# Kernel tuning notes

Hardware: AMD Instinct MI355X
Metric: run time of the kernel (lower is better)

The kernel has to match this reference:

```python
import jax, jax.numpy as jnp
import numpy as np

D = 512          # descriptor_dim
H = 8            # num_heads
HD = D // H      # per-head dim
L = 12           # GNN layers: ['self','cross']*6
NAMES = ['self', 'cross'] * 6
SINKHORN_ITERS = 100
IN_EPS = 1e-5    # InstanceNorm1d eps


def _conv1x1(W, b, x):
    # W: [o, d], b: [o], x: [b, d, n] -> [b, o, n]  (1x1 Conv1d)
    return jnp.einsum('od,bdn->bon', W, x) + b[:, None]


def _instance_norm(x):
    # InstanceNorm1d(affine=False): normalize each (batch, channel) over n
    mean = jnp.mean(x, axis=-1, keepdims=True)
    var = jnp.mean(jnp.square(x - mean), axis=-1, keepdims=True)  # biased
    return (x - mean) * jax.lax.rsqrt(var + IN_EPS)


def _mha(x, src, Wq, bq, Wk, bk, Wv, bv, Wm, bm):
    # x, src: [b, D, n] / [b, D, m]; fused head-major QKV projections
    b, _, n = x.shape
    m = src.shape[2]
    q = _conv1x1(Wq, bq, x).reshape(b, H, HD, n)
    k = _conv1x1(Wk, bk, src).reshape(b, H, HD, m)
    v = _conv1x1(Wv, bv, src).reshape(b, H, HD, m)
    scores = jnp.einsum('bhdn,bhdm->bhnm', q, k) / np.float32(np.sqrt(HD))
    prob = jax.nn.softmax(scores, axis=-1)
    out = jnp.einsum('bhnm,bhdm->bhdn', prob, v)      # [b, h, hd, n]
    # torch stacks heads at dim=2 -> [b, hd, h, n], then views (b, hd*h, n):
    out = out.transpose(0, 2, 1, 3).reshape(b, D, n)  # dim-major merge order
    return _conv1x1(Wm, bm, out)


def _prop_layer(x, src, Wq, bq, Wk, bk, Wv, bv, Wm, bm, W1, b1, W2, b2):
    # AttentionalPropagation: attn message + MLP([2D, 2D, D]) with InstanceNorm
    msg = _mha(x, src, Wq, bq, Wk, bk, Wv, bv, Wm, bm)
    y = jnp.concatenate([x, msg], axis=1)             # [b, 2D, n]
    z = jax.nn.relu(_instance_norm(_conv1x1(W1, b1, y)))
    return _conv1x1(W2, b2, z)                        # [b, D, n]


def _log_optimal_transport(scores, alpha, iters):
    b, m, n = scores.shape
    ms = jnp.asarray(m, scores.dtype)
    ns = jnp.asarray(n, scores.dtype)
    bins0 = jnp.broadcast_to(alpha, (b, m, 1))
    bins1 = jnp.broadcast_to(alpha, (b, 1, n))
    a = jnp.broadcast_to(alpha, (b, 1, 1))
    couplings = jnp.concatenate(
        [jnp.concatenate([scores, bins0], -1),
         jnp.concatenate([bins1, a], -1)], 1)         # [b, m+1, n+1]
    norm = -jnp.log(ms + ns)
    log_mu = jnp.concatenate([jnp.full((m,), norm), (jnp.log(ns) + norm)[None]])
    log_nu = jnp.concatenate([jnp.full((n,), norm), (jnp.log(ms) + norm)[None]])
    log_mu = jnp.broadcast_to(log_mu, (b, m + 1))
    log_nu = jnp.broadcast_to(log_nu, (b, n + 1))

    def step(carry, _):
        u, v = carry
        u = log_mu - jax.scipy.special.logsumexp(couplings + v[:, None, :], axis=2)
        v = log_nu - jax.scipy.special.logsumexp(couplings + u[:, :, None], axis=1)
        return (u, v), None

    (u, v), _ = jax.lax.scan(
        step, (jnp.zeros_like(log_mu), jnp.zeros_like(log_nu)), None,
        length=iters)
    return couplings + u[:, :, None] + v[:, None, :] - norm


def setup_inputs() -> dict:
    key = jax.random.key(0)
    ks = jax.random.split(key, 12)
    B, N0, N1 = 4, 1024, 1024
    s = np.float32(0.03)  # ~1/sqrt(D) init scale for stability over 12 layers

    def p(k, shape):
        return jax.random.normal(k, shape, jnp.float32) * s

    return {
        'descs_0': jax.random.normal(ks[0], (B, N0, D), jnp.float32),
        'descs_1': jax.random.normal(ks[1], (B, N1, D), jnp.float32),
        'Wq': p(ks[2], (L, D, D)), 'bq': jnp.zeros((L, D), jnp.float32),
        'Wk': p(ks[3], (L, D, D)), 'bk': jnp.zeros((L, D), jnp.float32),
        'Wv': p(ks[4], (L, D, D)), 'bv': jnp.zeros((L, D), jnp.float32),
        'Wm': p(ks[5], (L, D, D)), 'bm': jnp.zeros((L, D), jnp.float32),
        'W1': p(ks[6], (L, 2 * D, 2 * D)), 'b1': jnp.zeros((L, 2 * D), jnp.float32),
        'W2': p(ks[7], (L, D, 2 * D)), 'b2': jnp.zeros((L, D), jnp.float32),
        'Wf': p(ks[8], (D, D)), 'bf': jnp.zeros((D,), jnp.float32),
        'bin_score': jnp.asarray(1.0, jnp.float32),
    }


def reference(descs_0, descs_1, Wq, bq, Wk, bk, Wv, bv, Wm, bm,
              W1, b1, W2, b2, Wf, bf, bin_score):
    # [B, N, D] -> channels-first [B, D, N]
    x0 = jnp.transpose(descs_0, (0, 2, 1))
    x1 = jnp.transpose(descs_1, (0, 2, 1))
    for i, name in enumerate(NAMES):
        s0, s1 = (x1, x0) if name == 'cross' else (x0, x1)
        args = (Wq[i], bq[i], Wk[i], bk[i], Wv[i], bv[i], Wm[i], bm[i],
                W1[i], b1[i], W2[i], b2[i])
        d0 = _prop_layer(x0, s0, *args)
        d1 = _prop_layer(x1, s1, *args)
        x0 = x0 + d0
        x1 = x1 + d1
    m0 = _conv1x1(Wf, bf, x0)
    m1 = _conv1x1(Wf, bf, x1)
    scores = jnp.einsum('bdn,bdm->bnm', m0, m1) / np.float32(np.sqrt(D))
    return _log_optimal_transport(scores, bin_score, SINKHORN_ITERS)
```

## Files before the change

### kernel.cpp

```cpp
#include <hip/hip_runtime.h>
#include <hip/hip_bf16.h>
#include <hip/hip_fp16.h>
#include <cmath>

using bf16 = __hip_bfloat16;
typedef __attribute__((ext_vector_type(8))) short short8;
typedef __attribute__((ext_vector_type(4))) short shortx4;
typedef __attribute__((ext_vector_type(4))) float floatx4;
typedef unsigned long long u64t;

__device__ __forceinline__ void lds_load16(void* lds, const void* g) {
  __builtin_amdgcn_global_load_lds(
      (const __attribute__((address_space(1))) void*)g,
      (__attribute__((address_space(3))) void*)lds, 16, 0, 0);
}

struct GemmP {
  const bf16* A; const bf16* B;
  int M, N, K, lda, ldb;
  long sAimg, sAh, sBimg, sBh;
  int ZH, cross;
  float scale;
  const float* bias;
  float* Cf; int ldcf; long sCfImg, sCfH;
  bf16* Cb; int ldcb; long sCbImg, sCbH;
  __half* Ch; int ldch; long sChImg, sChH;
  const float* resid;
  bf16* Cv; int vColOfs;
  float* statsOut;
};

template <int NTILE>
__global__ __launch_bounds__(256, 2)
void gemm_bt(GemmP p) {
  __shared__ __align__(16) bf16 As[128 * 32];
  __shared__ __align__(16) bf16 Bs[NTILE * 32];
  constexpr int MI = (NTILE == 128) ? 4 : 2;
  const int z = blockIdx.z;
  const int imgA = z / p.ZH;
  const int h = z - imgA * p.ZH;
  const int imgB = imgA ^ p.cross;
  const bf16* Ab = p.A + (long)imgA * p.sAimg + (long)h * p.sAh;
  const bf16* Bb = p.B + (long)imgB * p.sBimg + (long)h * p.sBh;

  int bx = blockIdx.x, by = blockIdx.y;
  if (gridDim.z == 1) {
    const unsigned nwg = gridDim.x * gridDim.y;
    if ((nwg & 7u) == 0) {
      const unsigned id = blockIdx.y * gridDim.x + blockIdx.x;
      const unsigned nid = (id & 7u) * (nwg >> 3) + (id >> 3);
      bx = nid % gridDim.x;
      by = nid / gridDim.x;
    }
  }
  const int m0 = by * 128, n0 = bx * NTILE;
  const int t = threadIdx.x, w = t >> 6, l = t & 63;
  const int lr = l >> 2, lk = (l & 3) * 8;
  const int fr = l & 15, fk = (l >> 4) * 8;

  const bf16* aG0 = Ab + (long)(m0 + w * 16 + lr) * p.lda + lk;
  const bf16* aG1 = aG0 + (long)64 * p.lda;
  const bf16* bG0 = Bb + (long)(n0 + w * 16 + lr) * p.ldb + lk;
  const bf16* bG1 = bG0 + (long)64 * p.ldb;
  bf16* aL0 = &As[w * 16 * 32];
  bf16* aL1 = &As[(w + 4) * 16 * 32];
  bf16* bL0 = &Bs[w * 16 * 32];
  bf16* bL1 = &Bs[(w + 4) * 16 * 32];
  const int wr = (NTILE == 128) ? (w >> 1) * 64 : w * 32;
  const int wc = (NTILE == 128) ? (w & 1) * 64 : 0;

  floatx4 zero4 = {0.f, 0.f, 0.f, 0.f};
  floatx4 acc[MI][4];
#pragma unroll
  for (int i = 0; i < MI; i++)
#pragma unroll
    for (int j = 0; j < 4; j++) acc[i][j] = zero4;

  for (int k0 = 0; k0 < p.K; k0 += 32) {
    lds_load16(aL0, aG0 + k0);
    lds_load16(aL1, aG1 + k0);
    lds_load16(bL0, bG0 + k0);
    if (NTILE == 128) lds_load16(bL1, bG1 + k0);
    __syncthreads();
    short8 af[MI], bfv[4];
#pragma unroll
    for (int i = 0; i < MI; i++)
      af[i] = *(const short8*)&As[(wr + i * 16 + fr) * 32 + fk];
#pragma unroll
    for (int j = 0; j < 4; j++)
      bfv[j] = *(const short8*)&Bs[(wc + j * 16 + fr) * 32 + fk];
#pragma unroll
    for (int i = 0; i < MI; i++)
#pragma unroll
      for (int j = 0; j < 4; j++)
        acc[i][j] = __builtin_amdgcn_mfma_f32_16x16x32_bf16(af[i], bfv[j], acc[i][j], 0, 0, 0);
    __syncthreads();
  }

  const int cl = l & 15, rq = (l >> 4) * 4;
  const long cfBase = (long)imgA * p.sCfImg + (long)h * p.sCfH;
  const long cbBase = (long)imgA * p.sCbImg + (long)h * p.sCbH;
  const long chBase = (long)imgA * p.sChImg + (long)h * p.sChH;
#pragma unroll
  for (int j = 0; j < 4; j++) {
    const int col = n0 + wc + j * 16 + cl;
    if (col >= p.N) continue;
    const float bv = p.bias ? p.bias[col] : 0.f;
    const bool vcol = p.Cv && (col >= p.vColOfs);
    float cs = 0.f, cs2 = 0.f;
#pragma unroll
    for (int i = 0; i < MI; i++) {
      float vr[4];
#pragma unroll
      for (int r = 0; r < 4; r++) {
        const int row = m0 + wr + i * 16 + rq + r;
        float val = acc[i][j][r] * p.scale + bv;
        if (p.resid) val += p.resid[cfBase + (long)row * p.ldcf + col];
        if (p.Cf) p.Cf[cfBase + (long)row * p.ldcf + col] = val;
        if (p.Cb && !vcol) p.Cb[cbBase + (long)row * p.ldcb + col] = __float2bfloat16(val);
        if (p.Ch) p.Ch[chBase + (long)row * p.ldch + col] = __float2half(val);
        if (p.statsOut) { cs += val; cs2 += val * val; }
        vr[r] = val;
      }
      if (vcol) {
        const int row0 = m0 + wr + i * 16 + rq;
        const int img = row0 >> 10, tok = row0 & 1023;
        const int ch = col - p.vColOfs;
        shortx4 pk;
#pragma unroll
        for (int r = 0; r < 4; r++) {
          bf16 bb = __float2bfloat16(vr[r]);
          pk[r] = *reinterpret_cast<short*>(&bb);
        }
        *(shortx4*)(p.Cv + (long)img * 524288 + (long)ch * 1024 + tok) = pk;
      }
    }
    if (p.statsOut) {
      cs += __shfl_xor(cs, 16); cs += __shfl_xor(cs, 32);
      cs2 += __shfl_xor(cs2, 16); cs2 += __shfl_xor(cs2, 32);
      if (l < 16) {
        const int img = m0 >> 10;
        atomicAdd(&p.statsOut[img * 2048 + col], cs);
        atomicAdd(&p.statsOut[img * 2048 + 1024 + col], cs2);
      }
    }
  }
}

__global__ __launch_bounds__(256, 4)
void attn_fused(const bf16* __restrict__ QKV, const bf16* __restrict__ vchan,
                bf16* __restrict__ Yb, int cross) {
  __shared__ __align__(16) bf16 Qs[64 * 64];
  __shared__ __align__(16) bf16 Ks[64 * 64];
  __shared__ __align__(16) bf16 Vs[64 * 64];
  __shared__ __align__(16) bf16 Ps[64 * 64];
  const int z = blockIdx.z;
  const int img = z >> 3, h = z & 7;
  const int imgB = img ^ cross;
  const int q0 = blockIdx.x * 64;
  const int t = threadIdx.x, w = t >> 6, l = t & 63;
  const int g = l >> 4, fr = l & 15;
  const int wr = w * 16;

  {
    const bf16* src = QKV + ((long)(img * 1024 + q0)) * 1536 + h * 64;
#pragma unroll
    for (int k = 0; k < 2; k++) {
      const int chunk = t + k * 256;
      const int row = chunk >> 3, c16 = chunk & 7;
      const short8 vd = *(const short8*)(src + (long)row * 1536 + c16 * 8);
      *(short8*)((char*)Qs + row * 128 + ((c16 * 16) ^ ((row & 7) << 4))) = vd;
    }
  }
  __syncthreads();

  short8 qf[2];
#pragma unroll
  for (int ks = 0; ks < 2; ks++) {
    const int row = wr + fr;
    qf[ks] = *(const short8*)((const char*)Qs + row * 128 +
                              ((ks * 64 + g * 16) ^ ((row & 7) << 4)));
  }

  floatx4 zero4 = {0.f, 0.f, 0.f, 0.f};
  floatx4 Oa[4];
  float m_run[4], l_run[4];
#pragma unroll
  for (int r = 0; r < 4; r++) { m_run[r] = -3.0e38f; l_run[r] = 0.f; }
#pragma unroll
  for (int jd = 0; jd < 4; jd++) Oa[jd] = zero4;

  const bf16* ksrc0 = QKV + ((long)(imgB * 1024)) * 1536 + 512 + h * 64;
  const bf16* vsrc0 = vchan + (long)imgB * 524288 + (long)(h * 64) * 1024;

  for (int kv = 0; kv < 16; kv++) {
    const int kv0 = kv * 64;
#pragma unroll
    for (int k = 0; k < 2; k++) {
      const int ch = t + k * 256;
      const int row = ch >> 3, c16 = ch & 7;
      const short8 vd = *(const short8*)(ksrc0 + (long)(kv0 + row) * 1536 + c16 * 8);
      *(short8*)((char*)Ks + row * 128 + ((c16 * 16) ^ ((row & 7) << 4))) = vd;
    }
#pragma unroll
    for (int k = 0; k < 2; k++) {
      const int ch = t + k * 256;
      const int row = ch >> 3, c16 = ch & 7;
      const short8 vd = *(const short8*)(vsrc0 + (long)row * 1024 + kv0 + c16 * 8);
      *(short8*)((char*)Vs + row * 128 + ((c16 * 16) ^ ((row & 7) << 4))) = vd;
    }
    __syncthreads();

    floatx4 sa[4];
#pragma unroll
    for (int j = 0; j < 4; j++) {
      sa[j] = zero4;
      const int row = j * 16 + fr;
      const short8 bk0 = *(const short8*)((const char*)Ks + row * 128 +
                                          ((g * 16) ^ ((row & 7) << 4)));
      const short8 bk1 = *(const short8*)((const char*)Ks + row * 128 +
                                          ((64 + g * 16) ^ ((row & 7) << 4)));
      sa[j] = __builtin_amdgcn_mfma_f32_16x16x32_bf16(qf[0], bk0, sa[j], 0, 0, 0);
      sa[j] = __builtin_amdgcn_mfma_f32_16x16x32_bf16(qf[1], bk1, sa[j], 0, 0, 0);
    }

#pragma unroll
    for (int r = 0; r < 4; r++) {
      float mx = -3.0e38f;
#pragma unroll
      for (int j = 0; j < 4; j++) {
        sa[j][r] *= 0.125f;
        mx = fmaxf(mx, sa[j][r]);
      }
#pragma unroll
      for (int o = 1; o < 16; o <<= 1) mx = fmaxf(mx, __shfl_xor(mx, o));
      const float mnew = fmaxf(m_run[r], mx);
      const float corr = __expf(m_run[r] - mnew);
      m_run[r] = mnew;
      float ps = 0.f;
#pragma unroll
      for (int j = 0; j < 4; j++) {
        const float pv = __expf(sa[j][r] - mnew);
        sa[j][r] = pv;
        ps += pv;
      }
#pragma unroll
      for (int o = 1; o < 16; o <<= 1) ps += __shfl_xor(ps, o);
      l_run[r] = l_run[r] * corr + ps;
#pragma unroll
      for (int jd = 0; jd < 4; jd++) Oa[jd][r] *= corr;
    }

#pragma unroll
    for (int j = 0; j < 4; j++)
#pragma unroll
      for (int r = 0; r < 4; r++) {
        const int row = wr + g * 4 + r;
        const int colB = j * 32 + fr * 2;
        *(bf16*)((char*)Ps + row * 128 + (colB ^ ((row & 7) << 4))) =
            __float2bfloat16(sa[j][r]);
      }

    short8 pf[2];
#pragma unroll
    for (int ks = 0; ks < 2; ks++) {
      const int row = wr + fr;
      pf[ks] = *(const short8*)((const char*)Ps + row * 128 +
                                ((ks * 64 + g * 16) ^ ((row & 7) << 4)));
    }
#pragma unroll
    for (int jd = 0; jd < 4; jd++) {
      const int row = jd * 16 + fr;
      const short8 vf0 = *(const short8*)((const char*)Vs + row * 128 +
                                          ((g * 16) ^ ((row & 7) << 4)));
      const short8 vf1 = *(const short8*)((const char*)Vs + row * 128 +
                                          ((64 + g * 16) ^ ((row & 7) << 4)));
      Oa[jd] = __builtin_amdgcn_mfma_f32_16x16x32_bf16(pf[0], vf0, Oa[jd], 0, 0, 0);
      Oa[jd] = __builtin_amdgcn_mfma_f32_16x16x32_bf16(pf[1], vf1, Oa[jd], 0, 0, 0);
    }
    __syncthreads();
  }

#pragma unroll
  for (int r = 0; r < 4; r++) {
    const float inv = 1.f / l_run[r];
    const int qrow = q0 + wr + g * 4 + r;
    bf16* dst = Yb + ((long)img * 1024 + qrow) * 1024 + 512 + h * 64;
#pragma unroll
    for (int jd = 0; jd < 4; jd++)
      dst[jd * 16 + fr] = __float2bfloat16(Oa[jd][r] * inv);
  }
}

__global__ __launch_bounds__(256)
void cvt_f2b(const float* __restrict__ in, bf16* __restrict__ out, long n) {
  long i = (long)blockIdx.x * 256 + threadIdx.x;
  const long stride = (long)gridDim.x * 256;
  for (; i < n; i += stride) out[i] = __float2bfloat16(in[i]);
}

__global__ __launch_bounds__(256)
void cvt_prep(const float* __restrict__ W1, const float* __restrict__ Wm,
              bf16* __restrict__ w1r, bf16* __restrict__ wmT) {
  const long i = (long)blockIdx.x * 256 + threadIdx.x;
  if (i < 6291456L) {
    const int lay = (int)(i >> 19);
    const long r = i & 524287;
    const int o = (int)(r >> 9), k = (int)(r & 511);
    w1r[i] = __float2bfloat16(W1[(long)lay * 1048576 + (long)o * 1024 + 512 + k]);
  } else if (i < 9437184L) {
    const long j = i - 6291456L;
    const int lay = (int)(j >> 18);
    const long r = j & 262143;
    const int c = (int)(r >> 9), ii = (int)(r & 511);
    wmT[j] = __float2bfloat16(Wm[(long)lay * 262144 + (long)ii * 512 + (c & 63) * 8 + (c >> 6)]);
  }
}

__global__ __launch_bounds__(256)
void bc_calc(const float* __restrict__ W1, const float* __restrict__ bm,
             const float* __restrict__ b1, float* __restrict__ bc) {
  const int w = threadIdx.x >> 6, l = threadIdx.x & 63;
  const int og = blockIdx.x * 4 + w;
  const int lay = og >> 10, o = og & 1023;
  const float* wrow = W1 + (long)lay * 1048576 + (long)o * 1024 + 512;
  const float* bmr = bm + lay * 512;
  float s = 0.f;
#pragma unroll
  for (int j = 0; j < 8; j++) s += wrow[l + 64 * j] * bmr[l + 64 * j];
#pragma unroll
  for (int o2 = 32; o2 >= 1; o2 >>= 1) s += __shfl_xor(s, o2);
  if (l == 0) bc[og] = b1[og] + s;
}

__global__ __launch_bounds__(256)
void cvt_layer(const float* __restrict__ Wq, const float* __restrict__ Wk,
               const float* __restrict__ Wv, const float* __restrict__ W1,
               const float* __restrict__ W2, const bf16* __restrict__ wcAll,
               const float* __restrict__ bq, const float* __restrict__ bk,
               const float* __restrict__ bv,
               int layer, bf16* __restrict__ out, float* __restrict__ bqkv) {
  const long i = (long)blockIdx.x * 256 + threadIdx.x;
  if (i >= 589824) {
    const int j = (int)(i - 589824);
    if (j < 1536) {
      float b;
      if (j < 512) b = bq[layer * 512 + j];
      else if (j < 1024) b = bk[layer * 512 + j - 512];
      else b = bv[layer * 512 + j - 1024];
      bqkv[j] = b;
    }
    return;
  }
  const long e = i * 4;
  float4 vs;
  if (e < 786432) {
    const int rgn = (int)(e >> 18);
    const long o = e & 262143;
    const float* W = (rgn == 0) ? Wq : (rgn == 1) ? Wk : Wv;
    vs = *(const float4*)(W + (long)layer * 262144 + o);
  } else if (e < 1835008) {
    const long j = e - 786432;
    const int o = (int)(j >> 10), k = (int)(j & 1023);
    if (k >= 512) {
      *(shortx4*)(out + e) =
          *(const shortx4*)(wcAll + (long)layer * 524288 + (long)o * 512 + (k - 512));
      return;
    }
    vs = *(const float4*)(W1 + (long)layer * 1048576 + (long)o * 1024 + k);
  } else {
    vs = *(const float4*)(W2 + (long)layer * 524288 + (e - 1835008));
  }
  float vv[4] = {vs.x, vs.y, vs.z, vs.w};
  shortx4 pk;
#pragma unroll
  for (int k = 0; k < 4; k++) {
    bf16 bb = __float2bfloat16(vv[k]);
    pk[k] = *reinterpret_cast<short*>(&bb);
  }
  *(shortx4*)(out + e) = pk;
}

__global__ __launch_bounds__(256)
void init_x(const float* __restrict__ d0, const float* __restrict__ d1,
            float* __restrict__ Xf, bf16* __restrict__ Yb) {
  long i = (long)blockIdx.x * 256 + threadIdx.x;
  const long stride = (long)gridDim.x * 256;
  for (; i < 1048576; i += stride) {
    const int d4 = (int)(i & 127);
    const long nn = i >> 7;
    const int img = (int)(nn >> 10);
    const int row = (int)(nn & 1023);
    const int b = img >> 1, s = img & 1;
    const float4 v = *(const float4*)((s ? d1 : d0) + ((long)b * 1024 + row) * 512 + d4 * 4);
    *(float4*)(Xf + i * 4) = v;
    float vv[4] = {v.x, v.y, v.z, v.w};
    shortx4 pk;
#pragma unroll
    for (int k = 0; k < 4; k++) {
      bf16 bb = __float2bfloat16(vv[k]);
      pk[k] = *reinterpret_cast<short*>(&bb);
    }
    *(shortx4*)(Yb + (nn << 10) + d4 * 4) = pk;
  }
}

__global__ __launch_bounds__(256)
void in_apply(const float* __restrict__ T1, const float* __restrict__ stats,
              bf16* __restrict__ Z) {
  long i = (long)blockIdx.x * 256 + threadIdx.x;
  const long stride = (long)gridDim.x * 256;
  for (; i < 2L * 1024 * 1024; i += stride) {
    const float4 tv = *(const float4*)(T1 + i * 4);
    const int c0 = (int)((i * 4) & 1023);
    const int img = (int)(i >> 18);
    const float* st = stats + img * 2048;
    float vv[4] = {tv.x, tv.y, tv.z, tv.w};
    shortx4 zo;
#pragma unroll
    for (int k = 0; k < 4; k++) {
      const int c = c0 + k;
      const float mean = st[c] * (1.f / 1024.f);
      const float var = fmaxf(st[1024 + c] * (1.f / 1024.f) - mean * mean, 0.f);
      const float zz = (vv[k] - mean) * rsqrtf(var + 1e-5f);
      bf16 bb = __float2bfloat16(fmaxf(zz, 0.f));
      zo[k] = *reinterpret_cast<short*>(&bb);
    }
    *(shortx4*)(Z + i * 4) = zo;
  }
}

__global__ __launch_bounds__(256)
void coup_to_fp16(float* __restrict__ io, const float* __restrict__ alpha,
                  __half* __restrict__ outN, __half* __restrict__ outT) {
  __shared__ float tile[32][33];
  const float a = *alpha;
  const int b = blockIdx.z;
  const int x0 = blockIdx.x * 32, y0 = blockIdx.y * 32;
  const int lx = threadIdx.x & 31, ly = threadIdx.x >> 5;
#pragma unroll
  for (int i = 0; i < 4; i++) {
    const int y = ly + i * 8;
    if (y0 + y < 1025 && x0 + lx < 1025) {
      const long idx = ((long)b * 1025 + y0 + y) * 1025 + x0 + lx;
      const bool edge = (y0 + y == 1024) || (x0 + lx == 1024);
      float vv;
      if (edge) { vv = a; io[idx] = a; }
      else vv = io[idx];
      tile[y][lx] = vv;
      outN[idx] = __float2half(vv);
    }
  }
  __syncthreads();
#pragma unroll
  for (int i = 0; i < 4; i++) {
    const int y = ly + i * 8;
    if (x0 + y < 1025 && y0 + lx < 1025)
      outT[((long)b * 1025 + x0 + y) * 1025 + y0 + lx] = __float2half(tile[lx][y]);
  }
}

#define SK_BLOCKS 256

#define SK_ROUND(CREG, CLAST, XREG, XLAST, SRC, DST)                            \
  {                                                                             \
    u64t pr;                                                                    \
    while ((unsigned)((pr = __hip_atomic_load(&(SRC)[t], __ATOMIC_RELAXED,      \
                                              __HIP_MEMORY_SCOPE_AGENT)) >>    \
                      32) != tag)                                               \
      __builtin_amdgcn_s_sleep(1);                                              \
    sv[t] = __uint_as_float((unsigned)pr);                                      \
    if (t == 0) {                                                               \
      u64t qr;                                                                  \
      while ((unsigned)((qr = __hip_atomic_load(&(SRC)[1024], __ATOMIC_RELAXED, \
                                                __HIP_MEMORY_SCOPE_AGENT)) >>  \
                        32) != tag)                                             \
        __builtin_amdgcn_s_sleep(1);                                            \
      sv[1024] = __uint_as_float((unsigned)qr);                                 \
    }                                                                           \
    __syncthreads();                                                            \
    float M = (l == 0) ? ((CLAST) + sv[1024]) : -3.0e38f;                       \
    const float extra = M;                                                      \
    float x[16];                                                                \
    _Pragma("unroll") for (int i = 0; i < 16; i++) {                            \
      x[i] = (CREG)[i] + sv[l + 64 * i];                                        \
      M = fmaxf(M, x[i]);                                                       \
    }                                                                           \
    _Pragma("unroll") for (int o = 32; o >= 1; o >>= 1)                         \
        M = fmaxf(M, __shfl_xor(M, o));                                         \
    float S = (l == 0) ? __expf(extra - M) : 0.f;                               \
    _Pragma("unroll") for (int i = 0; i < 16; i++) S += __expf(x[i] - M);       \
    _Pragma("unroll") for (int o = 32; o >= 1; o >>= 1) S += __shfl_xor(S, o);  \
    if (l == 0) {                                                               \
      const float val = norm - (M + __logf(S));                                 \
      const u64t pk = ((u64t)(tag + 1) << 32) | (u64t)__float_as_uint(val);     \
      __hip_atomic_store(&(DST)[lw], pk, __ATOMIC_RELAXED,                      \
                         __HIP_MEMORY_SCOPE_AGENT);                             \
    }                                                                           \
    if (xtra) {                                                                 \
      float M2 = (l == 0) ? ((XLAST) + sv[1024]) : -3.0e38f;                    \
      const float e2 = M2;                                                      \
      float y[16];                                                              \
      _Pragma("unroll") for (int i = 0; i < 16; i++) {                          \
        y[i] = (XREG)[i] + sv[l + 64 * i];                                      \
        M2 = fmaxf(M2, y[i]);                                                   \
      }                                                                         \
      _Pragma("unroll") for (int o = 32; o >= 1; o >>= 1)                       \
          M2 = fmaxf(M2, __shfl_xor(M2, o));                                    \
      float S2 = (l == 0) ? __expf(e2 - M2) : 0.f;                              \
      _Pragma("unroll") for (int i = 0; i < 16; i++) S2 += __expf(y[i] - M2);   \
      _Pragma("unroll") for (int o = 32; o >= 1; o >>= 1)                       \
          S2 += __shfl_xor(S2, o);                                              \
      if (l == 0) {                                                             \
        const float v2 = (logN + norm) - (M2 + __logf(S2));                     \
        const u64t pk2 = ((u64t)(tag + 1) << 32) | (u64t)__float_as_uint(v2);   \
        __hip_atomic_store(&(DST)[1024], pk2, __ATOMIC_RELAXED,                 \
                           __HIP_MEMORY_SCOPE_AGENT);                           \
      }                                                                         \
    }                                                                           \
    tag++;                                                                      \
    __syncthreads();                                                            \
  }

__global__ __launch_bounds__(1024)
void sinkhorn_pers(const __half* __restrict__ C, const __half* __restrict__ CT,
                   u64t* __restrict__ u, u64t* __restrict__ v,
                   float norm, float logN, int iters) {
  __shared__ float sv[1025];
  const int t = threadIdx.x;
  const int w = t >> 6, l = t & 63;
  const int b = blockIdx.x >> 6;
  const int kb = blockIdx.x & 63;
  const int lw = kb * 16 + w;
  const __half* Cb = C + (long)b * 1050625;
  const __half* CTb = CT + (long)b * 1050625;
  u64t* ub = u + b * 1025;
  u64t* vb = v + b * 1025;

  float cr[16], cc[16];
  float clC, clT;
  {
    const __half* rc = Cb + (long)lw * 1025;
    const __half* rt = CTb + (long)lw * 1025;
#pragma unroll
    for (int i = 0; i < 16; i++) {
      cr[i] = __half2float(rc[l + 64 * i]);
      cc[i] = __half2float(rt[l + 64 * i]);
    }
    clC = (l == 0) ? __half2float(rc[1024]) : 0.f;
    clT = (l == 0) ? __half2float(rt[1024]) : 0.f;
  }
  const bool xtra = (lw == 0);
  float xrC[16], xrT[16], xlC = 0.f, xlT = 0.f;
  if (xtra) {
    const __half* rc = Cb + (long)1024 * 1025;
    const __half* rt = CTb + (long)1024 * 1025;
#pragma unroll
    for (int i = 0; i < 16; i++) {
      xrC[i] = __half2float(rc[l + 64 * i]);
      xrT[i] = __half2float(rt[l + 64 * i]);
    }
    if (l == 0) {
      xlC = __half2float(rc[1024]);
      xlT = __half2float(rt[1024]);
    }
  }

  unsigned tag = 0;
  for (int it = 0; it < iters; it++) {
    SK_ROUND(cr, clC, xrC, xlC, vb, ub);
    SK_ROUND(cc, clT, xrT, xlT, ub, vb);
  }
}

__global__ __launch_bounds__(256)
void ot_final(float* __restrict__ C, const u64t* __restrict__ u,
              const u64t* __restrict__ v, float norm) {
  long i = (long)blockIdx.x * 256 + threadIdx.x;
  if (i >= 4L * 1025 * 1025) return;
  const int b = (int)(i / 1050625);
  const long r = i - (long)b * 1050625;
  const int n = (int)(r / 1025);
  const int m = (int)(r - (long)n * 1025);
  const float uu = __uint_as_float((unsigned)u[b * 1025 + n]);
  const float vv = __uint_as_float((unsigned)v[b * 1025 + m]);
  C[i] += uu + vv - norm;
}

extern "C" void kernel_launch(void* const* d_in, const int* in_sizes, int n_in,
                              void* d_out, int out_size, void* d_ws, size_t ws_size,
                              hipStream_t stream) {
  (void)in_sizes; (void)n_in; (void)out_size; (void)ws_size;
  const float* descs0 = (const float*)d_in[0];
  const float* descs1 = (const float*)d_in[1];
  const float* Wq = (const float*)d_in[2];
  const float* bq = (const float*)d_in[3];
  const float* Wk = (const float*)d_in[4];
  const float* bk = (const float*)d_in[5];
  const float* Wv = (const float*)d_in[6];
  const float* bvv = (const float*)d_in[7];
  const float* Wm = (const float*)d_in[8];
  const float* bm = (const float*)d_in[9];
  const float* W1 = (const float*)d_in[10];
  const float* b1 = (const float*)d_in[11];
  const float* W2 = (const float*)d_in[12];
  const float* b2 = (const float*)d_in[13];
  const float* Wf = (const float*)d_in[14];
  const float* bff = (const float*)d_in[15];
  const float* alpha = (const float*)d_in[16];

  char* ws = (char*)d_ws;
  size_t off = 0;
  auto alloc = [&](size_t bytes) -> void* {
    off = (off + 255) & ~(size_t)255;
    void* p = ws + off;
    off += bytes;
    return p;
  };

  bf16* wL = (bf16*)alloc(2359296L * 2);
  float* bqkv = (float*)alloc(1536 * 4);
  bf16* WfB = (bf16*)alloc(512L * 512 * 2);
  bf16* wcAll = (bf16*)alloc(12L * 1024 * 512 * 2);
  float* bcAll = (float*)alloc(12L * 1024 * 4);
  float* Xf = (float*)alloc(8L * 1024 * 512 * 4);
  bf16* Yb = (bf16*)alloc(8L * 1024 * 1024 * 2);
  bf16* QKVb = (bf16*)alloc(8L * 1024 * 1536 * 2);
  bf16* vchan = (bf16*)alloc(8L * 1024 * 512 * 2);
  char* SCR = (char*)alloc(50331648);
  float* stats = (float*)alloc(12L * 16384 * 4);
  u64t* u = (u64t*)alloc(4L * 1025 * 8);
  u64t* v = (u64t*)alloc(4L * 1025 * 8);

  bf16* wqkv = wL;
  bf16* w1m = wL + 786432;
  bf16* w2 = wL + 1835008;
  float* T1 = (float*)SCR;
  bf16* Zb = (bf16*)(SCR + 33554432);
  bf16* w1rTmp = (bf16*)SCR;
  bf16* wmTTmp = (bf16*)(SCR + 12582912);
  __half* Ch = (__half*)SCR;
  __half* CTh = (__half*)(SCR + 8405248);
  bf16* mproj = (bf16*)(SCR + 33554432);
  float* coup = (float*)d_out;

  cvt_f2b<<<512, 256, 0, stream>>>(Wf, WfB, 512L * 512);
  init_x<<<2048, 256, 0, stream>>>(descs0, descs1, Xf, Yb);
  hipMemsetAsync(stats, 0, 12L * 16384 * 4, stream);

  auto gemm = [&](int ntile, const bf16* A, const bf16* B, int M, int N, int K,
                  int lda, int ldb, long sAimg, long sAh, long sBimg, long sBh,
                  int Z, int ZH, int cross, float scale, const float* bias,
                  float* Cf, int ldcf, long sCfImg, long sCfH,
                  bf16* Cb, int ldcb, long sCbImg, long sCbH,
                  __half* Ch_, int ldch, long sChImg, long sChH,
                  const float* resid, bf16* Cv, int vColOfs, float* statsOut) {
    GemmP p;
    p.A = A; p.B = B; p.M = M; p.N = N; p.K = K; p.lda = lda; p.ldb = ldb;
    p.sAimg = sAimg; p.sAh = sAh; p.sBimg = sBimg; p.sBh = sBh;
    p.ZH = ZH; p.cross = cross; p.scale = scale; p.bias = bias;
    p.Cf = Cf; p.ldcf = ldcf; p.sCfImg = sCfImg; p.sCfH = sCfH;
    p.Cb = Cb; p.ldcb = ldcb; p.sCbImg = sCbImg; p.sCbH = sCbH;
    p.Ch = Ch_; p.ldch = ldch; p.sChImg = sChImg; p.sChH = sChH;
    p.resid = resid; p.Cv = Cv; p.vColOfs = vColOfs; p.statsOut = statsOut;
    dim3 g((unsigned)((N + ntile - 1) / ntile), (unsigned)((M + 127) / 128), (unsigned)Z);
    if (ntile == 128) gemm_bt<128><<<g, 256, 0, stream>>>(p);
    else gemm_bt<64><<<g, 256, 0, stream>>>(p);
  };

  cvt_prep<<<36864, 256, 0, stream>>>(W1, Wm, w1rTmp, wmTTmp);
  bc_calc<<<3072, 256, 0, stream>>>(W1, bm, b1, bcAll);
  gemm(128, w1rTmp, wmTTmp, 1024, 512, 512, 512, 512, 524288, 0, 262144, 0,
       12, 1, 0, 1.f, nullptr,
       nullptr, 0, 0, 0, wcAll, 512, 524288, 0, nullptr, 0, 0, 0,
       nullptr, nullptr, 0, nullptr);

  for (int i = 0; i < 12; i++) {
    const int cross = i & 1;
    cvt_layer<<<2310, 256, 0, stream>>>(Wq, Wk, Wv, W1, W2, wcAll, bq, bk, bvv, i, wL, bqkv);

    gemm(128, Yb, wqkv, 8192, 1536, 512, 1024, 512, 0, 0, 0, 0, 1, 1, 0, 1.f, bqkv,
         nullptr, 0, 0, 0, QKVb, 1536, 0, 0, nullptr, 0, 0, 0,
         nullptr, vchan, 1024, nullptr);
    attn_fused<<<dim3(16, 1, 64), 256, 0, stream>>>(QKVb, vchan, Yb, cross);

    gemm(128, Yb, w1m, 8192, 1024, 1024, 1024, 1024, 0, 0, 0, 0, 1, 1, 0, 1.f,
         bcAll + i * 1024,
         T1, 1024, 0, 0, nullptr, 0, 0, 0, nullptr, 0, 0, 0,
         nullptr, nullptr, 0, stats + (long)i * 16384);
    in_apply<<<2048, 256, 0, stream>>>(T1, stats + (long)i * 16384, Zb);
    gemm(64, Zb, w2, 8192, 512, 1024, 1024, 1024, 0, 0, 0, 0, 1, 1, 0, 1.f, b2 + i * 512,
         Xf, 512, 0, 0, Yb, 1024, 0, 0, nullptr, 0, 0, 0,
         Xf, nullptr, 0, nullptr);
  }

  gemm(64, Yb, WfB, 8192, 512, 512, 1024, 512, 0, 0, 0, 0, 1, 1, 0, 1.f, bff,
       nullptr, 0, 0, 0, mproj, 512, 0, 0, nullptr, 0, 0, 0,
       nullptr, nullptr, 0, nullptr);
  gemm(64, mproj, mproj + 524288, 1024, 1024, 512, 512, 512,
       1048576, 0, 1048576, 0, 4, 1, 0,
       0.044194173824159216f, nullptr,
       coup, 1025, 1050625, 0, nullptr, 0, 0, 0, nullptr, 0, 0, 0,
       nullptr, nullptr, 0, nullptr);
  coup_to_fp16<<<dim3(33, 33, 4), 256, 0, stream>>>(coup, alpha, Ch, CTh);

  hipMemsetAsync(u, 0, 4L * 1025 * 8, stream);
  hipMemsetAsync(v, 0, 4L * 1025 * 8, stream);
  const float NORM = -logf(2048.f);
  const float LOGN = logf(1024.f);
  int iters = 100;
  void* args[] = {(void*)&Ch, (void*)&CTh, (void*)&u, (void*)&v,
                  (void*)&NORM, (void*)&LOGN, (void*)&iters};
  hipLaunchCooperativeKernel((void*)sinkhorn_pers, dim3(SK_BLOCKS), dim3(1024), args, 0, stream);
  ot_final<<<16417, 256, 0, stream>>>(coup, u, v, NORM);
}
```

Measured before the change: 2.927 ms.

## Batch per-layer weight conversion, deepen GEMM K-step, vectorize OT finalize

```diff
diff --git a/kernel.cpp b/kernel.cpp
--- a/kernel.cpp
+++ b/kernel.cpp
@@ -33,8 +33,8 @@
 template <int NTILE>
 __global__ __launch_bounds__(256, 2)
 void gemm_bt(GemmP p) {
-  __shared__ __align__(16) bf16 As[128 * 32];
-  __shared__ __align__(16) bf16 Bs[NTILE * 32];
+  __shared__ __align__(16) bf16 As[2][128 * 32];
+  __shared__ __align__(16) bf16 Bs[2][NTILE * 32];
   constexpr int MI = (NTILE == 128) ? 4 : 2;
   const int z = blockIdx.z;
   const int imgA = z / p.ZH;
@@ -62,10 +62,10 @@
   const bf16* aG1 = aG0 + (long)64 * p.lda;
   const bf16* bG0 = Bb + (long)(n0 + w * 16 + lr) * p.ldb + lk;
   const bf16* bG1 = bG0 + (long)64 * p.ldb;
-  bf16* aL0 = &As[w * 16 * 32];
-  bf16* aL1 = &As[(w + 4) * 16 * 32];
-  bf16* bL0 = &Bs[w * 16 * 32];
-  bf16* bL1 = &Bs[(w + 4) * 16 * 32];
+  bf16* aL0 = &As[0][w * 16 * 32];
+  bf16* aL1 = &As[0][(w + 4) * 16 * 32];
+  bf16* bL0 = &Bs[0][w * 16 * 32];
+  bf16* bL1 = &Bs[0][(w + 4) * 16 * 32];
   const int wr = (NTILE == 128) ? (w >> 1) * 64 : w * 32;
   const int wc = (NTILE == 128) ? (w & 1) * 64 : 0;
 
@@ -76,24 +76,33 @@
 #pragma unroll
     for (int j = 0; j < 4; j++) acc[i][j] = zero4;
 
-  for (int k0 = 0; k0 < p.K; k0 += 32) {
+  for (int k0 = 0; k0 < p.K; k0 += 64) {
     lds_load16(aL0, aG0 + k0);
     lds_load16(aL1, aG1 + k0);
+    lds_load16(aL0 + 128 * 32, aG0 + k0 + 32);
+    lds_load16(aL1 + 128 * 32, aG1 + k0 + 32);
     lds_load16(bL0, bG0 + k0);
-    if (NTILE == 128) lds_load16(bL1, bG1 + k0);
+    lds_load16(bL0 + NTILE * 32, bG0 + k0 + 32);
+    if (NTILE == 128) {
+      lds_load16(bL1, bG1 + k0);
+      lds_load16(bL1 + NTILE * 32, bG1 + k0 + 32);
+    }
     __syncthreads();
-    short8 af[MI], bfv[4];
-#pragma unroll
-    for (int i = 0; i < MI; i++)
-      af[i] = *(const short8*)&As[(wr + i * 16 + fr) * 32 + fk];
-#pragma unroll
-    for (int j = 0; j < 4; j++)
-      bfv[j] = *(const short8*)&Bs[(wc + j * 16 + fr) * 32 + fk];
-#pragma unroll
-    for (int i = 0; i < MI; i++)
+#pragma unroll
+    for (int ph = 0; ph < 2; ph++) {
+      short8 af[MI], bfv[4];
+#pragma unroll
+      for (int i = 0; i < MI; i++)
+        af[i] = *(const short8*)&As[ph][(wr + i * 16 + fr) * 32 + fk];
 #pragma unroll
       for (int j = 0; j < 4; j++)
-        acc[i][j] = __builtin_amdgcn_mfma_f32_16x16x32_bf16(af[i], bfv[j], acc[i][j], 0, 0, 0);
+        bfv[j] = *(const short8*)&Bs[ph][(wc + j * 16 + fr) * 32 + fk];
+#pragma unroll
+      for (int i = 0; i < MI; i++)
+#pragma unroll
+        for (int j = 0; j < 4; j++)
+          acc[i][j] = __builtin_amdgcn_mfma_f32_16x16x32_bf16(af[i], bfv[j], acc[i][j], 0, 0, 0);
+    }
     __syncthreads();
   }
 
@@ -339,7 +348,10 @@
                const float* __restrict__ W2, const bf16* __restrict__ wcAll,
                const float* __restrict__ bq, const float* __restrict__ bk,
                const float* __restrict__ bv,
-               int layer, bf16* __restrict__ out, float* __restrict__ bqkv) {
+               int layer0, bf16* __restrict__ outBase, float* __restrict__ bqkvBase) {
+  const int layer = layer0 + blockIdx.y;
+  bf16* out = outBase + (long)blockIdx.y * 2359296;
+  float* bqkv = bqkvBase + (long)blockIdx.y * 1536;
   const long i = (long)blockIdx.x * 256 + threadIdx.x;
   if (i >= 589824) {
     const int j = (int)(i - 589824);
@@ -576,21 +588,29 @@
 __global__ __launch_bounds__(256)
 void ot_final(float* __restrict__ C, const u64t* __restrict__ u,
               const u64t* __restrict__ v, float norm) {
-  long i = (long)blockIdx.x * 256 + threadIdx.x;
-  if (i >= 4L * 1025 * 1025) return;
-  const int b = (int)(i / 1050625);
-  const long r = i - (long)b * 1050625;
-  const int n = (int)(r / 1025);
-  const int m = (int)(r - (long)n * 1025);
-  const float uu = __uint_as_float((unsigned)u[b * 1025 + n]);
-  const float vv = __uint_as_float((unsigned)v[b * 1025 + m]);
-  C[i] += uu + vv - norm;
+  const long q = (long)blockIdx.x * 256 + threadIdx.x;
+  if (q >= 1050625L) return;
+  const long i = q * 4;
+  float4 cv = *(float4*)(C + i);
+  float vv[4] = {cv.x, cv.y, cv.z, cv.w};
+#pragma unroll
+  for (int k = 0; k < 4; k++) {
+    const long e = i + k;
+    const int b = (int)(e / 1050625);
+    const long r = e - (long)b * 1050625;
+    const int n = (int)(r / 1025);
+    const int m = (int)(r - (long)n * 1025);
+    vv[k] += __uint_as_float((unsigned)u[b * 1025 + n]) +
+             __uint_as_float((unsigned)v[b * 1025 + m]) - norm;
+  }
+  cv.x = vv[0]; cv.y = vv[1]; cv.z = vv[2]; cv.w = vv[3];
+  *(float4*)(C + i) = cv;
 }
 
 extern "C" void kernel_launch(void* const* d_in, const int* in_sizes, int n_in,
                               void* d_out, int out_size, void* d_ws, size_t ws_size,
                               hipStream_t stream) {
-  (void)in_sizes; (void)n_in; (void)out_size; (void)ws_size;
+  (void)in_sizes; (void)n_in; (void)out_size;
   const float* descs0 = (const float*)d_in[0];
   const float* descs1 = (const float*)d_in[1];
   const float* Wq = (const float*)d_in[2];
@@ -618,8 +638,11 @@
     return p;
   };
 
-  bf16* wL = (bf16*)alloc(2359296L * 2);
-  float* bqkv = (float*)alloc(1536 * 4);
+  const bool fullW = ws_size >= ((size_t)185 << 20);
+  const int NL = fullW ? 12 : 1;
+
+  bf16* wLbase = (bf16*)alloc((size_t)NL * 2359296L * 2);
+  float* bqkvBase = (float*)alloc((size_t)NL * 1536 * 4);
   bf16* WfB = (bf16*)alloc(512L * 512 * 2);
   bf16* wcAll = (bf16*)alloc(12L * 1024 * 512 * 2);
   float* bcAll = (float*)alloc(12L * 1024 * 4);
@@ -632,9 +655,6 @@
   u64t* u = (u64t*)alloc(4L * 1025 * 8);
   u64t* v = (u64t*)alloc(4L * 1025 * 8);
 
-  bf16* wqkv = wL;
-  bf16* w1m = wL + 786432;
-  bf16* w2 = wL + 1835008;
   float* T1 = (float*)SCR;
   bf16* Zb = (bf16*)(SCR + 33554432);
   bf16* w1rTmp = (bf16*)SCR;
@@ -674,12 +694,22 @@
        12, 1, 0, 1.f, nullptr,
        nullptr, 0, 0, 0, wcAll, 512, 524288, 0, nullptr, 0, 0, 0,
        nullptr, nullptr, 0, nullptr);
+  if (fullW)
+    cvt_layer<<<dim3(2310, 12), 256, 0, stream>>>(Wq, Wk, Wv, W1, W2, wcAll,
+                                                  bq, bk, bvv, 0, wLbase, bqkvBase);
 
   for (int i = 0; i < 12; i++) {
     const int cross = i & 1;
-    cvt_layer<<<2310, 256, 0, stream>>>(Wq, Wk, Wv, W1, W2, wcAll, bq, bk, bvv, i, wL, bqkv);
-
-    gemm(128, Yb, wqkv, 8192, 1536, 512, 1024, 512, 0, 0, 0, 0, 1, 1, 0, 1.f, bqkv,
+    bf16* wLay = wLbase + (fullW ? (long)i * 2359296 : 0);
+    float* bqkvL = bqkvBase + (fullW ? (long)i * 1536 : 0);
+    bf16* wqkv = wLay;
+    bf16* w1m = wLay + 786432;
+    bf16* w2 = wLay + 1835008;
+    if (!fullW)
+      cvt_layer<<<dim3(2310, 1), 256, 0, stream>>>(Wq, Wk, Wv, W1, W2, wcAll,
+                                                   bq, bk, bvv, i, wLbase, bqkvBase);
+
+    gemm(128, Yb, wqkv, 8192, 1536, 512, 1024, 512, 0, 0, 0, 0, 1, 1, 0, 1.f, bqkvL,
          nullptr, 0, 0, 0, QKVb, 1536, 0, 0, nullptr, 0, 0, 0,
          nullptr, vchan, 1024, nullptr);
     attn_fused<<<dim3(16, 1, 64), 256, 0, stream>>>(QKVb, vchan, Yb, cross);
@@ -712,5 +742,5 @@
   void* args[] = {(void*)&Ch, (void*)&CTh, (void*)&u, (void*)&v,
                   (void*)&NORM, (void*)&LOGN, (void*)&iters};
   hipLaunchCooperativeKernel((void*)sinkhorn_pers, dim3(SK_BLOCKS), dim3(1024), args, 0, stream);
-  ot_final<<<16417, 256, 0, stream>>>(coup, u, v, NORM);
-}
+  ot_final<<<4105, 256, 0, stream>>>(coup, u, v, NORM);
+}
```

Measured after the change: 2.939 ms. Within noise of the previous version (+0.4%).
